# Performance work log

Measured on AMD Instinct MI355X. Metric: run time of the kernel, lower is better.

## Reference

```python
import jax, jax.numpy as jnp
import numpy as np

NEG = -1e9  # finite stand-in for -inf (avoids inf-inf NaNs, safe in fp32)


def setup_inputs() -> dict:
    T, V, Lmax, A = 2048, 8192, 8, 64
    rng = np.random.default_rng(0)
    seq = rng.integers(0, A, size=T).astype(np.int32)
    # first A pieces are the single codepoints -> every sequence is segmentable
    piece_lens = np.concatenate([
        np.ones(A, np.int32),
        rng.integers(1, Lmax + 1, size=V - A).astype(np.int32),
    ])
    pieces = rng.integers(0, A, size=(V, Lmax)).astype(np.int32)
    pieces[:A, 0] = np.arange(A)
    logits = rng.standard_normal(V).astype(np.float32)
    m = logits.max()
    log_probs = (logits - m - np.log(np.exp(logits - m).sum())).astype(np.float32)
    return {
        'seq': jnp.asarray(seq),
        'pieces': jnp.asarray(pieces),
        'piece_lens': jnp.asarray(piece_lens),
        'log_probs': jnp.asarray(log_probs),
    }


def reference(seq, pieces, piece_lens, log_probs):
    T = seq.shape[0]
    V, Lmax = pieces.shape
    dt = log_probs.dtype

    # --- match table: match[t, i] = piece i matches sequence at position t ---
    seq_pad = jnp.concatenate([seq, jnp.full((Lmax,), -1, seq.dtype)])
    windows = seq_pad[jnp.arange(T)[:, None] + jnp.arange(Lmax)[None, :]]  # [T, Lmax]
    lmask = jnp.arange(Lmax)[None, :] < piece_lens[:, None]                # [V, Lmax]
    eq = windows[:, None, :] == pieces[None, :, :]                        # [T, V, Lmax]
    fits = (jnp.arange(T)[:, None] + piece_lens[None, :]) <= T            # [T, V]
    match = jnp.all(eq | ~lmask[None, :, :], axis=-1) & fits              # [T, V]
    mlp = jnp.where(match, log_probs[None, :], NEG).astype(dt)            # [T, V]

    # end_logp[t-1, i] = mlp[t - len_i, i]  (piece i ending exactly at t, t=1..T)
    te = jnp.arange(1, T + 1)[:, None]
    src = te - piece_lens[None, :]
    end_logp = jnp.where(src >= 0,
                         mlp[jnp.clip(src, 0, T - 1), jnp.arange(V)[None, :]],
                         NEG)

    # --- forward pass: alpha[t] = logsumexp_i alpha[t - len_i] + log p_i ---
    idx_a = Lmax - piece_lens  # window slot holding alpha[t - len_i]
    def fstep(win, row):
        a_t = jax.nn.logsumexp(win[idx_a] + row)
        return jnp.concatenate([win[1:], a_t[None]]), a_t
    win0 = jnp.full((Lmax,), NEG, dt).at[-1].set(0.0)
    _, alpha_rest = jax.lax.scan(fstep, win0, end_logp)
    alpha = jnp.concatenate([jnp.zeros((1,), dt), alpha_rest])  # [T+1]

    # --- backward pass: beta[t] = logsumexp_i log p_i + beta[t + len_i] ---
    idx_b = piece_lens - 1  # window slot holding beta[t + len_i]
    def bstep(win, row):
        b_t = jax.nn.logsumexp(row + win[idx_b])
        return jnp.concatenate([b_t[None], win[:-1]]), b_t
    winT = jnp.full((Lmax,), NEG, dt).at[0].set(0.0)
    _, beta_rev = jax.lax.scan(bstep, winT, mlp[::-1])
    beta = jnp.concatenate([beta_rev[::-1], jnp.zeros((1,), dt)])  # [T+1]

    # --- posteriors: P[t, i] = exp(alpha[t] + log p_i + beta[t+len_i] - alpha[T]) ---
    norm = alpha[T]
    beta_next = beta[jnp.clip(jnp.arange(T)[:, None] + piece_lens[None, :], 0, T)]
    P = jnp.exp(alpha[:T][:, None] + mlp + beta_next - norm)
    P = jnp.where(match, P, 0.0)
    return jnp.where(norm > NEG / 2, P, jnp.zeros_like(P))
```

## Files before the change

kernel.cpp:

```cpp
#include <hip/hip_runtime.h>
#include <stdint.h>

#define LMAX 8
#define KCH 32
#define NC  64
#define TT  2048
#define LN2D 0.6931471805599453
#define NEGE (-(1<<28))
#define VG 4

__device__ __forceinline__ int fexp(float m) { return ((__float_as_int(m) >> 23) & 0xFF) - 127; }
__device__ __forceinline__ int fexpbits(float m) { return (__float_as_int(m) >> 23) & 0xFF; }
__device__ __forceinline__ float p2(int e) { return __int_as_float((e + 127) << 23); }
__device__ __forceinline__ float p2c(int e) { return (e < -126) ? 0.f : p2(e); }

__global__ __launch_bounds__(256) void k_front(const int* __restrict__ seq,
        const int* __restrict__ pieces, const int* __restrict__ plens,
        const float* __restrict__ logp, float* __restrict__ Mpart, int T, int V) {
  __shared__ int sSeq[40];
  __shared__ unsigned long long sw[32];
  __shared__ float sM[32][8];
  const int tid = threadIdx.x;
  const int g = blockIdx.x;
  const int c = blockIdx.y;
  const int base = c * KCH;

  if (tid < 40) {
    int pos = base + tid;
    sSeq[tid] = (pos < T) ? (seq[pos] & 0xFF) : 0xFF;
  }
  ((float*)sM)[tid] = 0.f;
  __syncthreads();
  if (tid < 32) {
    unsigned long long w = 0ull;
    #pragma unroll
    for (int l = 0; l < LMAX; ++l)
      w |= (unsigned long long)sSeq[tid + l] << (8 * l);
    sw[tid] = w;
  }
  __syncthreads();

  for (int r = 0; r < 8; ++r) {
    int v = (g * 8 + r) * 256 + tid;
    const int4* pr = (const int4*)(pieces + v * LMAX);
    int4 pa = pr[0], pb = pr[1];
    int len = plens[v];
    unsigned long long key = 0ull;
    if (0 < len) key |= (unsigned long long)(pa.x & 0xFF);
    if (1 < len) key |= (unsigned long long)(pa.y & 0xFF) << 8;
    if (2 < len) key |= (unsigned long long)(pa.z & 0xFF) << 16;
    if (3 < len) key |= (unsigned long long)(pa.w & 0xFF) << 24;
    if (4 < len) key |= (unsigned long long)(pb.x & 0xFF) << 32;
    if (5 < len) key |= (unsigned long long)(pb.y & 0xFF) << 40;
    if (6 < len) key |= (unsigned long long)(pb.z & 0xFF) << 48;
    if (7 < len) key |= (unsigned long long)(pb.w & 0xFF) << 56;
    unsigned long long mask = (len >= 8) ? ~0ull : ((1ull << (8 * len)) - 1ull);
    float prob = -1.f;
    #pragma unroll
    for (int t = 0; t < 32; ++t) {
      if (((sw[t] ^ key) & mask) == 0ull) {
        if (prob < 0.f) prob = expf(logp[v]);
        atomicAdd(&sM[t][len - 1], prob);
      }
    }
  }
  __syncthreads();
  if (tid < 64) ((float4*)Mpart)[((size_t)g * NC + c) * 64 + tid] = ((float4*)sM)[tid];
}

__global__ __launch_bounds__(1024, 1) void k_back(const float* __restrict__ Mpart,
        float* M, float* __restrict__ Pm, float* __restrict__ aL, float* __restrict__ bL) {
  __shared__ float sWt[128][68];
  __shared__ int   sEW[128 * 8];
  __shared__ int   sEP[128 * 8];
  __shared__ float Gm[16 * 69];
  __shared__ float Sg[16 * 9];
  __shared__ int   EGs[16 * 8];
  __shared__ int   EsB[16];
  __shared__ float sCs[128 * 8];
  __shared__ int   sEacc[128];
  const int tid = threadIdx.x;

  {
    const float4* Mp = (const float4*)Mpart;
    float4* M4 = (float4*)M;
    for (int i = tid; i < 4096; i += 1024) {
      float4 a = Mp[i];
      float4 b = Mp[4096 + i];
      float4 cc = Mp[8192 + i];
      float4 d = Mp[12288 + i];
      float4 s;
      s.x = (a.x + b.x) + (cc.x + d.x);
      s.y = (a.y + b.y) + (cc.y + d.y);
      s.z = (a.z + b.z) + (cc.z + d.z);
      s.w = (a.w + b.w) + (cc.w + d.w);
      M4[i] = s;
    }
  }
  __syncthreads();
  const float4* Mv = (const float4*)M;

  {
    int task = tid >> 3, b = tid & 7;
    int dir = task >> 6, c = task & 63;
    int base = c * KCH;
    float v[8];
    #pragma unroll
    for (int i = 0; i < 8; ++i) v[i] = (i == b) ? 1.f : 0.f;
    int ec = 0;
    if (dir == 0) {
      float4 ra = Mv[base * 2], rb = Mv[base * 2 + 1];
      for (int kg = 0; kg < 4; ++kg) {
        #pragma unroll
        for (int kk = 0; kk < 8; ++kk) {
          int k = kg * 8 + kk;
          float4 c0 = ra, c1 = rb;
          int nk = (k + 1 < KCH) ? k + 1 : KCH - 1;
          ra = Mv[(base + nk) * 2]; rb = Mv[(base + nk) * 2 + 1];
          float a_ = v[kk & 7];
          v[(kk + 1) & 7] = fmaf(a_, c0.x, v[(kk + 1) & 7]);
          v[(kk + 2) & 7] = fmaf(a_, c0.y, v[(kk + 2) & 7]);
          v[(kk + 3) & 7] = fmaf(a_, c0.z, v[(kk + 3) & 7]);
          v[(kk + 4) & 7] = fmaf(a_, c0.w, v[(kk + 4) & 7]);
          v[(kk + 5) & 7] = fmaf(a_, c1.x, v[(kk + 5) & 7]);
          v[(kk + 6) & 7] = fmaf(a_, c1.y, v[(kk + 6) & 7]);
          v[(kk + 7) & 7] = fmaf(a_, c1.z, v[(kk + 7) & 7]);
          v[kk & 7]       = a_ * c1.w;
          if (kk == 3 || kk == 7) {
            float mx = 0.f;
            #pragma unroll
            for (int i = 0; i < 8; ++i) mx = fmaxf(mx, v[i]);
            if (fexpbits(mx) != 0) {
              int e = fexp(mx); float sc = p2(-e);
              #pragma unroll
              for (int i = 0; i < 8; ++i) v[i] *= sc;
              ec += e;
            }
          }
        }
      }
    } else {
      float4 ra = Mv[(base + KCH - 1) * 2], rb = Mv[(base + KCH - 1) * 2 + 1];
      for (int kg = 0; kg < 4; ++kg) {
        #pragma unroll
        for (int kk = 0; kk < 8; ++kk) {
          int k = kg * 8 + kk;
          float4 c0 = ra, c1 = rb;
          int nk = (k + 1 < KCH) ? k + 1 : KCH - 1;
          int nt = base + KCH - 1 - nk;
          ra = Mv[nt * 2]; rb = Mv[nt * 2 + 1];
          float nb =      c0.x * v[(8  - kk) & 7];
          nb = fmaf(c0.y, v[(9  - kk) & 7], nb);
          nb = fmaf(c0.z, v[(10 - kk) & 7], nb);
          nb = fmaf(c0.w, v[(11 - kk) & 7], nb);
          nb = fmaf(c1.x, v[(12 - kk) & 7], nb);
          nb = fmaf(c1.y, v[(13 - kk) & 7], nb);
          nb = fmaf(c1.z, v[(14 - kk) & 7], nb);
          nb = fmaf(c1.w, v[(15 - kk) & 7], nb);
          v[(7 - kk) & 7] = nb;
          if (kk == 3 || kk == 7) {
            float mx = 0.f;
            #pragma unroll
            for (int i = 0; i < 8; ++i) mx = fmaxf(mx, v[i]);
            if (fexpbits(mx) != 0) {
              int e = fexp(mx); float sc = p2(-e);
              #pragma unroll
              for (int i = 0; i < 8; ++i) v[i] *= sc;
              ec += e;
            }
          }
        }
      }
    }
    float mx = 0.f;
    #pragma unroll
    for (int i = 0; i < 8; ++i) mx = fmaxf(mx, v[i]);
    int lt = dir * 64 + (dir ? 63 - c : c);
    if (fexpbits(mx) == 0) {
      #pragma unroll
      for (int i = 0; i < 8; ++i) sWt[lt][b * 8 + i] = 0.f;
      sEW[lt * 8 + b] = NEGE;
    } else {
      int e = fexp(mx); float sc = p2(-e);
      #pragma unroll
      for (int i = 0; i < 8; ++i) sWt[lt][b * 8 + i] = v[i] * sc;
      sEW[lt * 8 + b] = ec + e;
    }
  }
  __syncthreads();

  if (tid < 128) {
    const int dir = tid >> 6, w = (tid >> 3) & 7, b = tid & 7;
    float v[8];
    #pragma unroll
    for (int i = 0; i < 8; ++i) v[i] = (i == b) ? 1.f : 0.f;
    int ec = 0;
    for (int c = 0; c < 8; ++c) {
      int lc = w * 8 + c, lt = dir * 64 + lc;
      float* pp = Pm + lt * 64 + b * 8;
      #pragma unroll
      for (int i = 0; i < 8; ++i) pp[i] = v[i];
      sEP[lt * 8 + b] = ec;
      const float* wp = &sWt[lt][0];
      int ew[8];
      #pragma unroll
      for (int j = 0; j < 8; ++j) ew[j] = sEW[lt * 8 + j];
      int emax = ew[0];
      #pragma unroll
      for (int j = 1; j < 8; ++j) emax = max(emax, ew[j]);
      float nv[8] = {0, 0, 0, 0, 0, 0, 0, 0};
      #pragma unroll
      for (int j = 0; j < 8; ++j) {
        float tj = v[j] * p2c(ew[j] - emax + 64);
        float4 ca = *(const float4*)(wp + j * 8);
        float4 cb = *(const float4*)(wp + j * 8 + 4);
        nv[0] = fmaf(tj, ca.x, nv[0]); nv[1] = fmaf(tj, ca.y, nv[1]);
        nv[2] = fmaf(tj, ca.z, nv[2]); nv[3] = fmaf(tj, ca.w, nv[3]);
        nv[4] = fmaf(tj, cb.x, nv[4]); nv[5] = fmaf(tj, cb.y, nv[5]);
        nv[6] = fmaf(tj, cb.z, nv[6]); nv[7] = fmaf(tj, cb.w, nv[7]);
      }
      float mx = 0.f;
      #pragma unroll
      for (int i = 0; i < 8; ++i) mx = fmaxf(mx, nv[i]);
      if (fexpbits(mx) == 0) {
        #pragma unroll
        for (int i = 0; i < 8; ++i) v[i] = 0.f;
        ec = NEGE;
      } else {
        int e = fexp(mx); float sc = p2(-e);
        #pragma unroll
        for (int i = 0; i < 8; ++i) v[i] = nv[i] * sc;
        ec = ec + emax + e - 64;
      }
    }
    float* gp = Gm + (dir * 8 + w) * 69 + b * 8;
    #pragma unroll
    for (int i = 0; i < 8; ++i) gp[i] = v[i];
    EGs[(dir * 8 + w) * 8 + b] = ec;
  }
  __syncthreads();

  if (tid < 8 || (tid >= 64 && tid < 72)) {
    const int dir = (tid >= 64) ? 1 : 0, j = tid & 7;
    float s[8];
    #pragma unroll
    for (int i = 0; i < 8; ++i) s[i] = (i == 0) ? 1.f : 0.f;
    int Es = 0;
    for (int w = 0; w < 8; ++w) {
      float sj = s[0];
      #pragma unroll
      for (int i = 1; i < 8; ++i) if (j == i) sj = s[i];
      Sg[(dir * 8 + w) * 9 + j] = sj;
      if (j == 0) EsB[dir * 8 + w] = Es;
      int eg[8];
      #pragma unroll
      for (int i = 0; i < 8; ++i) eg[i] = EGs[(dir * 8 + w) * 8 + i];
      int egmax = eg[0];
      #pragma unroll
      for (int i = 1; i < 8; ++i) egmax = max(egmax, eg[i]);
      int egj = eg[0];
      #pragma unroll
      for (int i = 1; i < 8; ++i) if (j == i) egj = eg[i];
      float tb = sj * p2c(egj - egmax + 64);
      const float* gp = Gm + (dir * 8 + w) * 69 + j * 8;
      float p[8];
      #pragma unroll
      for (int i = 0; i < 8; ++i) p[i] = gp[i] * tb;
      #pragma unroll
      for (int m = 1; m <= 4; m <<= 1)
        #pragma unroll
        for (int i = 0; i < 8; ++i) p[i] += __shfl_xor(p[i], m);
      float mx = 0.f;
      #pragma unroll
      for (int i = 0; i < 8; ++i) mx = fmaxf(mx, p[i]);
      int e = fexp(mx); float sc = p2(-e);
      #pragma unroll
      for (int i = 0; i < 8; ++i) s[i] = p[i] * sc;
      Es += egmax + e - 64;
    }
  }
  __syncthreads();

  if (tid < 128) {
    const int dir = tid >> 6, lc = tid & 63, w = lc >> 3;
    float sg[8];
    #pragma unroll
    for (int b = 0; b < 8; ++b) sg[b] = Sg[(dir * 8 + w) * 9 + b];
    int Es = EsB[dir * 8 + w];
    int ep[8];
    #pragma unroll
    for (int b = 0; b < 8; ++b) ep[b] = sEP[(dir * 64 + lc) * 8 + b];
    int epmax = ep[0];
    #pragma unroll
    for (int b = 1; b < 8; ++b) epmax = max(epmax, ep[b]);
    float cs[8] = {0, 0, 0, 0, 0, 0, 0, 0};
    #pragma unroll
    for (int b = 0; b < 8; ++b) {
      float coef = sg[b] * p2c(ep[b] - epmax + 64);
      const float* pp = Pm + (dir * 64 + lc) * 64 + b * 8;
      float4 ca = *(const float4*)pp;
      float4 cb = *(const float4*)(pp + 4);
      cs[0] = fmaf(coef, ca.x, cs[0]); cs[1] = fmaf(coef, ca.y, cs[1]);
      cs[2] = fmaf(coef, ca.z, cs[2]); cs[3] = fmaf(coef, ca.w, cs[3]);
      cs[4] = fmaf(coef, cb.x, cs[4]); cs[5] = fmaf(coef, cb.y, cs[5]);
      cs[6] = fmaf(coef, cb.z, cs[6]); cs[7] = fmaf(coef, cb.w, cs[7]);
    }
    float mx = 0.f;
    #pragma unroll
    for (int i = 0; i < 8; ++i) mx = fmaxf(mx, cs[i]);
    int phys = dir ? (63 - lc) : lc;
    float* cp = &sCs[(dir * 64 + phys) * 8];
    if (fexpbits(mx) == 0) {
      #pragma unroll
      for (int i = 0; i < 8; ++i) cp[i] = 0.f;
      sEacc[dir * 64 + phys] = NEGE;
    } else {
      int e = fexp(mx); float sc = p2(-e);
      #pragma unroll
      for (int i = 0; i < 8; ++i) cp[i] = cs[i] * sc;
      sEacc[dir * 64 + phys] = Es + epmax + e - 64;
    }
  }
  __syncthreads();

  if (tid < 128) {
    const int dir = tid >> 6;
    const int c = tid & 63;
    const int base = c * KCH;
    const float* cp = &sCs[(dir * 64 + c) * 8];
    double st[8];
    #pragma unroll
    for (int i = 0; i < 8; ++i) st[i] = (double)cp[i];
    const double eacc = (double)sEacc[dir * 64 + c];
    if (tid == 0) { aL[0] = 0.f; bL[TT] = 0.f; }
    if (dir == 0) {
      float4 ra = Mv[base * 2], rb = Mv[base * 2 + 1];
      for (int kg = 0; kg < 4; ++kg) {
        #pragma unroll
        for (int kk = 0; kk < 8; ++kk) {
          int k = kg * 8 + kk;
          float4 c0 = ra, c1 = rb;
          int nk = (k + 1 < KCH) ? k + 1 : KCH - 1;
          ra = Mv[(base + nk) * 2]; rb = Mv[(base + nk) * 2 + 1];
          double a_ = st[kk & 7];
          st[(kk + 1) & 7] = fma(a_, (double)c0.x, st[(kk + 1) & 7]);
          st[(kk + 2) & 7] = fma(a_, (double)c0.y, st[(kk + 2) & 7]);
          st[(kk + 3) & 7] = fma(a_, (double)c0.z, st[(kk + 3) & 7]);
          st[(kk + 4) & 7] = fma(a_, (double)c0.w, st[(kk + 4) & 7]);
          st[(kk + 5) & 7] = fma(a_, (double)c1.x, st[(kk + 5) & 7]);
          st[(kk + 6) & 7] = fma(a_, (double)c1.y, st[(kk + 6) & 7]);
          st[(kk + 7) & 7] = fma(a_, (double)c1.z, st[(kk + 7) & 7]);
          st[kk & 7]       = a_ * (double)c1.w;
          double val = st[(kk + 1) & 7];
          long long bits = __double_as_longlong(val);
          int e2 = (int)((bits >> 52) & 0x7ff) - 1023;
          double mant = __longlong_as_double((bits & 0xFFFFFFFFFFFFFLL) | 0x3FF0000000000000LL);
          float lg = log2f((float)mant);
          aL[base + k + 1] = (float)(((double)e2 + eacc + (double)lg) * LN2D);
        }
      }
    } else {
      float4 ra = Mv[(base + KCH - 1) * 2], rb = Mv[(base + KCH - 1) * 2 + 1];
      for (int kg = 0; kg < 4; ++kg) {
        #pragma unroll
        for (int kk = 0; kk < 8; ++kk) {
          int k = kg * 8 + kk;
          int t = base + KCH - 1 - k;
          float4 c0 = ra, c1 = rb;
          int nk = (k + 1 < KCH) ? k + 1 : KCH - 1;
          int nt = base + KCH - 1 - nk;
          ra = Mv[nt * 2]; rb = Mv[nt * 2 + 1];
          double nb =            (double)c0.x * st[(8  - kk) & 7];
          nb = fma((double)c0.y, st[(9  - kk) & 7], nb);
          nb = fma((double)c0.z, st[(10 - kk) & 7], nb);
          nb = fma((double)c0.w, st[(11 - kk) & 7], nb);
          nb = fma((double)c1.x, st[(12 - kk) & 7], nb);
          nb = fma((double)c1.y, st[(13 - kk) & 7], nb);
          nb = fma((double)c1.z, st[(14 - kk) & 7], nb);
          nb = fma((double)c1.w, st[(15 - kk) & 7], nb);
          st[(7 - kk) & 7] = nb;
          long long bits = __double_as_longlong(nb);
          int e2 = (int)((bits >> 52) & 0x7ff) - 1023;
          double mant = __longlong_as_double((bits & 0xFFFFFFFFFFFFFLL) | 0x3FF0000000000000LL);
          float lg = log2f((float)mant);
          bL[t] = (float)(((double)e2 + eacc + (double)lg) * LN2D);
        }
      }
    }
  }
}

__global__ __launch_bounds__(256) void k_out(const int* __restrict__ seq,
        const int* __restrict__ pieces, const int* __restrict__ plens,
        const float* __restrict__ logp, const float* __restrict__ aL,
        const float* __restrict__ bL, float* __restrict__ out, int T, int V) {
  __shared__ int sSeq[40];
  __shared__ unsigned long long sw[32];
  const int tid = threadIdx.x;
  const int t0 = blockIdx.y * 32;
  const int v0 = blockIdx.x * 1024 + tid * 4;
  if (tid < 40) {
    int pos = t0 + tid;
    sSeq[tid] = (pos < T) ? (seq[pos] & 0xFF) : 0xFF;
  }
  __syncthreads();
  if (tid < 32) {
    unsigned long long w = 0ull;
    #pragma unroll
    for (int l = 0; l < LMAX; ++l)
      w |= (unsigned long long)sSeq[tid + l] << (8 * l);
    sw[tid] = w;
  }
  __syncthreads();

  float norm = aL[T];
  unsigned long long key[4], mask[4];
  int len[4];
  float lpb[4];
  #pragma unroll
  for (int j = 0; j < 4; ++j) {
    int v = v0 + j;
    const int4* pr = (const int4*)(pieces + v * LMAX);
    int4 pa = pr[0], pb = pr[1];
    int ln = plens[v];
    unsigned long long k_ = 0ull;
    if (0 < ln) k_ |= (unsigned long long)(pa.x & 0xFF);
    if (1 < ln) k_ |= (unsigned long long)(pa.y & 0xFF) << 8;
    if (2 < ln) k_ |= (unsigned long long)(pa.z & 0xFF) << 16;
    if (3 < ln) k_ |= (unsigned long long)(pa.w & 0xFF) << 24;
    if (4 < ln) k_ |= (unsigned long long)(pb.x & 0xFF) << 32;
    if (5 < ln) k_ |= (unsigned long long)(pb.y & 0xFF) << 40;
    if (6 < ln) k_ |= (unsigned long long)(pb.z & 0xFF) << 48;
    if (7 < ln) k_ |= (unsigned long long)(pb.w & 0xFF) << 56;
    key[j] = k_;
    mask[j] = (ln >= 8) ? ~0ull : ((1ull << (8 * ln)) - 1ull);
    len[j] = ln;
    lpb[j] = logp[v] - norm;
  }

  for (int tt = 0; tt < 32; ++tt) {
    int t = t0 + tt;
    unsigned long long w = sw[tt];
    float al = aL[t];
    float4 o = make_float4(0.f, 0.f, 0.f, 0.f);
    if (((w ^ key[0]) & mask[0]) == 0ull) o.x = __expf(al + lpb[0] + bL[t + len[0]]);
    if (((w ^ key[1]) & mask[1]) == 0ull) o.y = __expf(al + lpb[1] + bL[t + len[1]]);
    if (((w ^ key[2]) & mask[2]) == 0ull) o.z = __expf(al + lpb[2] + bL[t + len[2]]);
    if (((w ^ key[3]) & mask[3]) == 0ull) o.w = __expf(al + lpb[3] + bL[t + len[3]]);
    *(float4*)&out[(size_t)t * V + v0] = o;
  }
}

extern "C" void kernel_launch(void* const* d_in, const int* in_sizes, int n_in,
                              void* d_out, int out_size, void* d_ws, size_t ws_size,
                              hipStream_t stream) {
  const int* seq    = (const int*)d_in[0];
  const int* pieces = (const int*)d_in[1];
  const int* plens  = (const int*)d_in[2];
  const float* logp = (const float*)d_in[3];
  float* out = (float*)d_out;
  const int T = in_sizes[0];
  const int V = in_sizes[2];

  char* p = (char*)d_ws;
  float* Mpart = (float*)p;  p += (size_t)VG * NC * KCH * LMAX * 4;
  float* M = (float*)p;      p += (size_t)TT * LMAX * 4;
  float* Pm = (float*)p;     p += (size_t)128 * 64 * 4;
  float* aL = (float*)p;     p += 8208;
  float* bL = (float*)p;     p += 8208;

  dim3 g1(VG, NC);
  k_front<<<g1, 256, 0, stream>>>(seq, pieces, plens, logp, Mpart, T, V);
  k_back<<<1, 1024, 0, stream>>>(Mpart, M, Pm, aL, bL);
  dim3 g3(V / 1024, T / 32);
  k_out<<<g3, 256, 0, stream>>>(seq, pieces, plens, logp, aL, bL, out, T, V);
}
```

Baseline: 68.02 us.

## Split single-block scan kernel into per-chunk, combine, and replay kernels

The monolithic single-workgroup k_back, which reduced partial match sums and ran the chunked forward/backward scan, is split into three kernels. k_mat runs one block per chunk and does the partial-sum reduction and the chunk transfer matrices in parallel across 64 blocks. k_comb does the sequential combine in one block, and k_rep replays the chunks in two blocks, one per direction. Chunk rows are now preloaded into register buffers instead of software-prefetched one row at a time. This adds two extra kernel launches and global-memory round trips for the intermediates, in exchange for spreading the matrix stage across CUs.

```diff
diff --git a/kernel.cpp b/kernel.cpp
--- a/kernel.cpp
+++ b/kernel.cpp
@@ -68,55 +68,46 @@
   if (tid < 64) ((float4*)Mpart)[((size_t)g * NC + c) * 64 + tid] = ((float4*)sM)[tid];
 }
 
-__global__ __launch_bounds__(1024, 1) void k_back(const float* __restrict__ Mpart,
-        float* M, float* __restrict__ Pm, float* __restrict__ aL, float* __restrict__ bL) {
-  __shared__ float sWt[128][68];
-  __shared__ int   sEW[128 * 8];
-  __shared__ int   sEP[128 * 8];
-  __shared__ float Gm[16 * 69];
-  __shared__ float Sg[16 * 9];
-  __shared__ int   EGs[16 * 8];
-  __shared__ int   EsB[16];
-  __shared__ float sCs[128 * 8];
-  __shared__ int   sEacc[128];
+__global__ __launch_bounds__(64, 1) void k_mat(const float* __restrict__ Mpart,
+        float* __restrict__ M, float* __restrict__ Wt, int* __restrict__ EWc) {
+  __shared__ float sM[32][8];
   const int tid = threadIdx.x;
-
+  const int c = blockIdx.x;
   {
     const float4* Mp = (const float4*)Mpart;
-    float4* M4 = (float4*)M;
-    for (int i = tid; i < 4096; i += 1024) {
-      float4 a = Mp[i];
-      float4 b = Mp[4096 + i];
-      float4 cc = Mp[8192 + i];
-      float4 d = Mp[12288 + i];
-      float4 s;
-      s.x = (a.x + b.x) + (cc.x + d.x);
-      s.y = (a.y + b.y) + (cc.y + d.y);
-      s.z = (a.z + b.z) + (cc.z + d.z);
-      s.w = (a.w + b.w) + (cc.w + d.w);
-      M4[i] = s;
-    }
-  }
-  __syncthreads();
-  const float4* Mv = (const float4*)M;
-
-  {
-    int task = tid >> 3, b = tid & 7;
-    int dir = task >> 6, c = task & 63;
-    int base = c * KCH;
+    float4 a  = Mp[((size_t)(0 * NC + c)) * 64 + tid];
+    float4 b  = Mp[((size_t)(1 * NC + c)) * 64 + tid];
+    float4 cc = Mp[((size_t)(2 * NC + c)) * 64 + tid];
+    float4 d  = Mp[((size_t)(3 * NC + c)) * 64 + tid];
+    float4 s;
+    s.x = (a.x + b.x) + (cc.x + d.x);
+    s.y = (a.y + b.y) + (cc.y + d.y);
+    s.z = (a.z + b.z) + (cc.z + d.z);
+    s.w = (a.w + b.w) + (cc.w + d.w);
+    ((float4*)sM)[tid] = s;
+    ((float4*)M)[(size_t)c * 64 + tid] = s;
+  }
+  __syncthreads();
+
+  if (tid < 16) {
+    const int dir = tid >> 3, b = tid & 7;
     float v[8];
     #pragma unroll
     for (int i = 0; i < 8; ++i) v[i] = (i == b) ? 1.f : 0.f;
     int ec = 0;
+    float4 buf[32];
     if (dir == 0) {
-      float4 ra = Mv[base * 2], rb = Mv[base * 2 + 1];
-      for (int kg = 0; kg < 4; ++kg) {
-        #pragma unroll
-        for (int kk = 0; kk < 8; ++kk) {
-          int k = kg * 8 + kk;
-          float4 c0 = ra, c1 = rb;
-          int nk = (k + 1 < KCH) ? k + 1 : KCH - 1;
-          ra = Mv[(base + nk) * 2]; rb = Mv[(base + nk) * 2 + 1];
+      #pragma unroll
+      for (int half = 0; half < 2; ++half) {
+        #pragma unroll
+        for (int i = 0; i < 16; ++i) {
+          buf[2 * i]     = *(const float4*)&sM[half * 16 + i][0];
+          buf[2 * i + 1] = *(const float4*)&sM[half * 16 + i][4];
+        }
+        #pragma unroll
+        for (int i = 0; i < 16; ++i) {
+          const int kk = half * 16 + i;
+          float4 c0 = buf[2 * i], c1 = buf[2 * i + 1];
           float a_ = v[kk & 7];
           v[(kk + 1) & 7] = fmaf(a_, c0.x, v[(kk + 1) & 7]);
           v[(kk + 2) & 7] = fmaf(a_, c0.y, v[(kk + 2) & 7]);
@@ -126,29 +117,32 @@
           v[(kk + 6) & 7] = fmaf(a_, c1.y, v[(kk + 6) & 7]);
           v[(kk + 7) & 7] = fmaf(a_, c1.z, v[(kk + 7) & 7]);
           v[kk & 7]       = a_ * c1.w;
-          if (kk == 3 || kk == 7) {
+          if ((kk & 3) == 3) {
             float mx = 0.f;
             #pragma unroll
-            for (int i = 0; i < 8; ++i) mx = fmaxf(mx, v[i]);
+            for (int q = 0; q < 8; ++q) mx = fmaxf(mx, v[q]);
             if (fexpbits(mx) != 0) {
               int e = fexp(mx); float sc = p2(-e);
               #pragma unroll
-              for (int i = 0; i < 8; ++i) v[i] *= sc;
+              for (int q = 0; q < 8; ++q) v[q] *= sc;
               ec += e;
             }
           }
         }
       }
     } else {
-      float4 ra = Mv[(base + KCH - 1) * 2], rb = Mv[(base + KCH - 1) * 2 + 1];
-      for (int kg = 0; kg < 4; ++kg) {
-        #pragma unroll
-        for (int kk = 0; kk < 8; ++kk) {
-          int k = kg * 8 + kk;
-          float4 c0 = ra, c1 = rb;
-          int nk = (k + 1 < KCH) ? k + 1 : KCH - 1;
-          int nt = base + KCH - 1 - nk;
-          ra = Mv[nt * 2]; rb = Mv[nt * 2 + 1];
+      #pragma unroll
+      for (int half = 0; half < 2; ++half) {
+        #pragma unroll
+        for (int i = 0; i < 16; ++i) {
+          int row = 31 - (half * 16 + i);
+          buf[2 * i]     = *(const float4*)&sM[row][0];
+          buf[2 * i + 1] = *(const float4*)&sM[row][4];
+        }
+        #pragma unroll
+        for (int i = 0; i < 16; ++i) {
+          const int kk = half * 16 + i;
+          float4 c0 = buf[2 * i], c1 = buf[2 * i + 1];
           float nb =      c0.x * v[(8  - kk) & 7];
           nb = fmaf(c0.y, v[(9  - kk) & 7], nb);
           nb = fmaf(c0.z, v[(10 - kk) & 7], nb);
@@ -158,14 +152,14 @@
           nb = fmaf(c1.z, v[(14 - kk) & 7], nb);
           nb = fmaf(c1.w, v[(15 - kk) & 7], nb);
           v[(7 - kk) & 7] = nb;
-          if (kk == 3 || kk == 7) {
+          if ((kk & 3) == 3) {
             float mx = 0.f;
             #pragma unroll
-            for (int i = 0; i < 8; ++i) mx = fmaxf(mx, v[i]);
+            for (int q = 0; q < 8; ++q) mx = fmaxf(mx, v[q]);
             if (fexpbits(mx) != 0) {
               int e = fexp(mx); float sc = p2(-e);
               #pragma unroll
-              for (int i = 0; i < 8; ++i) v[i] *= sc;
+              for (int q = 0; q < 8; ++q) v[q] *= sc;
               ec += e;
             }
           }
@@ -176,20 +170,41 @@
     #pragma unroll
     for (int i = 0; i < 8; ++i) mx = fmaxf(mx, v[i]);
     int lt = dir * 64 + (dir ? 63 - c : c);
+    float* wp = Wt + lt * 64;
     if (fexpbits(mx) == 0) {
       #pragma unroll
-      for (int i = 0; i < 8; ++i) sWt[lt][b * 8 + i] = 0.f;
-      sEW[lt * 8 + b] = NEGE;
+      for (int i = 0; i < 8; ++i) wp[b * 8 + i] = 0.f;
+      EWc[lt * 8 + b] = NEGE;
     } else {
       int e = fexp(mx); float sc = p2(-e);
       #pragma unroll
-      for (int i = 0; i < 8; ++i) sWt[lt][b * 8 + i] = v[i] * sc;
-      sEW[lt * 8 + b] = ec + e;
-    }
-  }
-  __syncthreads();
-
-  if (tid < 128) {
+      for (int i = 0; i < 8; ++i) wp[b * 8 + i] = v[i] * sc;
+      EWc[lt * 8 + b] = ec + e;
+    }
+  }
+}
+
+__global__ __launch_bounds__(128, 1) void k_comb(const float* __restrict__ Wt,
+        const int* __restrict__ EWc, float* __restrict__ Pm,
+        float* __restrict__ Cs, int* __restrict__ Eacc) {
+  __shared__ float sWt[128][68];
+  __shared__ int   sEW[128 * 8];
+  __shared__ int   sEP[128 * 8];
+  __shared__ float Gm[16 * 69];
+  __shared__ float Sg[16 * 9];
+  __shared__ int   EGs[16 * 8];
+  __shared__ int   EsB[16];
+  const int tid = threadIdx.x;
+
+  for (int i = tid; i < 128 * 16; i += 128) {
+    int task = i >> 4, q = i & 15;
+    float4 v4 = ((const float4*)Wt)[i];
+    *(float4*)&sWt[task][q * 4] = v4;
+  }
+  for (int i = tid; i < 1024; i += 128) sEW[i] = EWc[i];
+  __syncthreads();
+
+  {
     const int dir = tid >> 6, w = (tid >> 3) & 7, b = tid & 7;
     float v[8];
     #pragma unroll
@@ -281,7 +296,7 @@
   }
   __syncthreads();
 
-  if (tid < 128) {
+  {
     const int dir = tid >> 6, lc = tid & 63, w = lc >> 3;
     float sg[8];
     #pragma unroll
@@ -309,82 +324,93 @@
     #pragma unroll
     for (int i = 0; i < 8; ++i) mx = fmaxf(mx, cs[i]);
     int phys = dir ? (63 - lc) : lc;
-    float* cp = &sCs[(dir * 64 + phys) * 8];
+    float* cp = Cs + (dir * 64 + phys) * 8;
     if (fexpbits(mx) == 0) {
       #pragma unroll
       for (int i = 0; i < 8; ++i) cp[i] = 0.f;
-      sEacc[dir * 64 + phys] = NEGE;
+      Eacc[dir * 64 + phys] = NEGE;
     } else {
       int e = fexp(mx); float sc = p2(-e);
       #pragma unroll
       for (int i = 0; i < 8; ++i) cp[i] = cs[i] * sc;
-      sEacc[dir * 64 + phys] = Es + epmax + e - 64;
-    }
-  }
-  __syncthreads();
-
-  if (tid < 128) {
-    const int dir = tid >> 6;
-    const int c = tid & 63;
-    const int base = c * KCH;
-    const float* cp = &sCs[(dir * 64 + c) * 8];
-    double st[8];
-    #pragma unroll
-    for (int i = 0; i < 8; ++i) st[i] = (double)cp[i];
-    const double eacc = (double)sEacc[dir * 64 + c];
-    if (tid == 0) { aL[0] = 0.f; bL[TT] = 0.f; }
-    if (dir == 0) {
-      float4 ra = Mv[base * 2], rb = Mv[base * 2 + 1];
-      for (int kg = 0; kg < 4; ++kg) {
-        #pragma unroll
-        for (int kk = 0; kk < 8; ++kk) {
-          int k = kg * 8 + kk;
-          float4 c0 = ra, c1 = rb;
-          int nk = (k + 1 < KCH) ? k + 1 : KCH - 1;
-          ra = Mv[(base + nk) * 2]; rb = Mv[(base + nk) * 2 + 1];
-          double a_ = st[kk & 7];
-          st[(kk + 1) & 7] = fma(a_, (double)c0.x, st[(kk + 1) & 7]);
-          st[(kk + 2) & 7] = fma(a_, (double)c0.y, st[(kk + 2) & 7]);
-          st[(kk + 3) & 7] = fma(a_, (double)c0.z, st[(kk + 3) & 7]);
-          st[(kk + 4) & 7] = fma(a_, (double)c0.w, st[(kk + 4) & 7]);
-          st[(kk + 5) & 7] = fma(a_, (double)c1.x, st[(kk + 5) & 7]);
-          st[(kk + 6) & 7] = fma(a_, (double)c1.y, st[(kk + 6) & 7]);
-          st[(kk + 7) & 7] = fma(a_, (double)c1.z, st[(kk + 7) & 7]);
-          st[kk & 7]       = a_ * (double)c1.w;
-          double val = st[(kk + 1) & 7];
-          long long bits = __double_as_longlong(val);
-          int e2 = (int)((bits >> 52) & 0x7ff) - 1023;
-          double mant = __longlong_as_double((bits & 0xFFFFFFFFFFFFFLL) | 0x3FF0000000000000LL);
-          float lg = log2f((float)mant);
-          aL[base + k + 1] = (float)(((double)e2 + eacc + (double)lg) * LN2D);
-        }
-      }
-    } else {
-      float4 ra = Mv[(base + KCH - 1) * 2], rb = Mv[(base + KCH - 1) * 2 + 1];
-      for (int kg = 0; kg < 4; ++kg) {
-        #pragma unroll
-        for (int kk = 0; kk < 8; ++kk) {
-          int k = kg * 8 + kk;
-          int t = base + KCH - 1 - k;
-          float4 c0 = ra, c1 = rb;
-          int nk = (k + 1 < KCH) ? k + 1 : KCH - 1;
-          int nt = base + KCH - 1 - nk;
-          ra = Mv[nt * 2]; rb = Mv[nt * 2 + 1];
-          double nb =            (double)c0.x * st[(8  - kk) & 7];
-          nb = fma((double)c0.y, st[(9  - kk) & 7], nb);
-          nb = fma((double)c0.z, st[(10 - kk) & 7], nb);
-          nb = fma((double)c0.w, st[(11 - kk) & 7], nb);
-          nb = fma((double)c1.x, st[(12 - kk) & 7], nb);
-          nb = fma((double)c1.y, st[(13 - kk) & 7], nb);
-          nb = fma((double)c1.z, st[(14 - kk) & 7], nb);
-          nb = fma((double)c1.w, st[(15 - kk) & 7], nb);
-          st[(7 - kk) & 7] = nb;
-          long long bits = __double_as_longlong(nb);
-          int e2 = (int)((bits >> 52) & 0x7ff) - 1023;
-          double mant = __longlong_as_double((bits & 0xFFFFFFFFFFFFFLL) | 0x3FF0000000000000LL);
-          float lg = log2f((float)mant);
-          bL[t] = (float)(((double)e2 + eacc + (double)lg) * LN2D);
-        }
+      Eacc[dir * 64 + phys] = Es + epmax + e - 64;
+    }
+  }
+}
+
+__global__ __launch_bounds__(64, 1) void k_rep(const float* __restrict__ M,
+        const float* __restrict__ Cs, const int* __restrict__ Eacc,
+        float* __restrict__ aL, float* __restrict__ bL) {
+  const int dir = blockIdx.x;
+  const int c = threadIdx.x;
+  const int base = c * KCH;
+  const float4* Mv = (const float4*)M;
+  const float* cp = Cs + (dir * 64 + c) * 8;
+  double st[8];
+  #pragma unroll
+  for (int i = 0; i < 8; ++i) st[i] = (double)cp[i];
+  const double eacc = (double)Eacc[dir * 64 + c];
+  float4 buf[32];
+  if (dir == 0) {
+    if (c == 0) aL[0] = 0.f;
+    #pragma unroll
+    for (int half = 0; half < 2; ++half) {
+      #pragma unroll
+      for (int i = 0; i < 16; ++i) {
+        int row = base + half * 16 + i;
+        buf[2 * i]     = Mv[row * 2];
+        buf[2 * i + 1] = Mv[row * 2 + 1];
+      }
+      #pragma unroll
+      for (int i = 0; i < 16; ++i) {
+        const int kk = half * 16 + i;
+        float4 c0 = buf[2 * i], c1 = buf[2 * i + 1];
+        double a_ = st[kk & 7];
+        st[(kk + 1) & 7] = fma(a_, (double)c0.x, st[(kk + 1) & 7]);
+        st[(kk + 2) & 7] = fma(a_, (double)c0.y, st[(kk + 2) & 7]);
+        st[(kk + 3) & 7] = fma(a_, (double)c0.z, st[(kk + 3) & 7]);
+        st[(kk + 4) & 7] = fma(a_, (double)c0.w, st[(kk + 4) & 7]);
+        st[(kk + 5) & 7] = fma(a_, (double)c1.x, st[(kk + 5) & 7]);
+        st[(kk + 6) & 7] = fma(a_, (double)c1.y, st[(kk + 6) & 7]);
+        st[(kk + 7) & 7] = fma(a_, (double)c1.z, st[(kk + 7) & 7]);
+        st[kk & 7]       = a_ * (double)c1.w;
+        double val = st[(kk + 1) & 7];
+        long long bits = __double_as_longlong(val);
+        int e2 = (int)((bits >> 52) & 0x7ff) - 1023;
+        double mant = __longlong_as_double((bits & 0xFFFFFFFFFFFFFLL) | 0x3FF0000000000000LL);
+        float lg = log2f((float)mant);
+        aL[base + kk + 1] = (float)(((double)e2 + eacc + (double)lg) * LN2D);
+      }
+    }
+  } else {
+    if (c == 0) bL[TT] = 0.f;
+    #pragma unroll
+    for (int half = 0; half < 2; ++half) {
+      #pragma unroll
+      for (int i = 0; i < 16; ++i) {
+        int row = base + 31 - (half * 16 + i);
+        buf[2 * i]     = Mv[row * 2];
+        buf[2 * i + 1] = Mv[row * 2 + 1];
+      }
+      #pragma unroll
+      for (int i = 0; i < 16; ++i) {
+        const int kk = half * 16 + i;
+        const int t = base + 31 - kk;
+        float4 c0 = buf[2 * i], c1 = buf[2 * i + 1];
+        double nb =            (double)c0.x * st[(8  - kk) & 7];
+        nb = fma((double)c0.y, st[(9  - kk) & 7], nb);
+        nb = fma((double)c0.z, st[(10 - kk) & 7], nb);
+        nb = fma((double)c0.w, st[(11 - kk) & 7], nb);
+        nb = fma((double)c1.x, st[(12 - kk) & 7], nb);
+        nb = fma((double)c1.y, st[(13 - kk) & 7], nb);
+        nb = fma((double)c1.z, st[(14 - kk) & 7], nb);
+        nb = fma((double)c1.w, st[(15 - kk) & 7], nb);
+        st[(7 - kk) & 7] = nb;
+        long long bits = __double_as_longlong(nb);
+        int e2 = (int)((bits >> 52) & 0x7ff) - 1023;
+        double mant = __longlong_as_double((bits & 0xFFFFFFFFFFFFFLL) | 0x3FF0000000000000LL);
+        float lg = log2f((float)mant);
+        bL[t] = (float)(((double)e2 + eacc + (double)lg) * LN2D);
       }
     }
   }
@@ -465,13 +491,19 @@
   char* p = (char*)d_ws;
   float* Mpart = (float*)p;  p += (size_t)VG * NC * KCH * LMAX * 4;
   float* M = (float*)p;      p += (size_t)TT * LMAX * 4;
+  float* Wt = (float*)p;     p += (size_t)128 * 64 * 4;
+  int* EWc = (int*)p;        p += (size_t)128 * 8 * 4;
   float* Pm = (float*)p;     p += (size_t)128 * 64 * 4;
+  float* Cs = (float*)p;     p += (size_t)128 * 8 * 4;
+  int* Eacc = (int*)p;       p += 512;
   float* aL = (float*)p;     p += 8208;
   float* bL = (float*)p;     p += 8208;
 
   dim3 g1(VG, NC);
   k_front<<<g1, 256, 0, stream>>>(seq, pieces, plens, logp, Mpart, T, V);
-  k_back<<<1, 1024, 0, stream>>>(Mpart, M, Pm, aL, bL);
+  k_mat<<<NC, 64, 0, stream>>>(Mpart, M, Wt, EWc);
+  k_comb<<<1, 128, 0, stream>>>(Wt, EWc, Pm, Cs, Eacc);
+  k_rep<<<2, 64, 0, stream>>>(M, Cs, Eacc, aL, bL);
   dim3 g3(V / 1024, T / 32);
   k_out<<<g3, 256, 0, stream>>>(seq, pieces, plens, logp, aL, bL, out, T, V);
 }
```

Measured after the change: 69.68 us. 1.02x slower.
